# Optimization experiments

Hardware: AMD Instinct MI355X
Metric: run time of the kernel (lower is better)

Reference implementation:

```python
import jax, jax.numpy as jnp
import numpy as np

HALF_LOG_2PI = 0.5 * float(np.log(2.0 * np.pi))


def setup_inputs() -> dict:
    key = jax.random.key(0)
    k1, k2 = jax.random.split(key)
    N, D = 16384, 2048
    x = jax.random.normal(k1, (N, D), dtype=jnp.float32)
    raw_params = jax.random.normal(k2, (2 * D,), dtype=jnp.float32)
    # chain spanning tree: edges (i, i+1) for i in 0..D-2  -> shape [D-1, 2]
    idx = jnp.arange(D - 1, dtype=jnp.int64)
    edges = jnp.stack([idx, idx + 1], axis=1)
    return {"x": x, "raw_params": raw_params, "edges": edges}


def reference(x, raw_params, edges):
    # x: [N, D] float; raw_params: [2D] float; edges: [E, 2] int
    D = x.shape[1]
    means = jnp.tanh(raw_params[:D]) * 2.0               # [D]
    stds = jax.nn.softplus(raw_params[D:]) + 1e-6         # [D]
    # Each edge (i, j) contributes logN(x_i) + logN(x_j); equivalently each
    # feature k contributes deg(k) * logN(x_k), deg = endpoint multiplicity.
    deg = jnp.zeros((D,), dtype=x.dtype).at[edges.reshape(-1)].add(1.0)  # [D]
    z = (x - means) / stds                                # [N, D]
    logp = -0.5 * z * z - jnp.log(stds) - HALF_LOG_2PI    # [N, D]
    return logp @ deg                                     # [N]
```

## Files before the change

kernel.cpp:

```cpp
#include <hip/hip_runtime.h>
#include <math.h>

#define HALF_LOG_2PI_F 0.9189385332046727f

typedef float f32x4 __attribute__((ext_vector_type(4)));

__global__ void clt_prep_kernel(const float* __restrict__ rp,
                                const int* __restrict__ edges,
                                float* __restrict__ A,
                                float* __restrict__ B,
                                float* __restrict__ csum,
                                int D, int E) {
    extern __shared__ float sdeg[];
    for (int k = threadIdx.x; k < D; k += blockDim.x) sdeg[k] = 0.0f;
    __syncthreads();
    for (int e = threadIdx.x; e < E; e += blockDim.x) {
        atomicAdd(&sdeg[edges[2 * e]], 1.0f);
        atomicAdd(&sdeg[edges[2 * e + 1]], 1.0f);
    }
    __syncthreads();
    float local_c = 0.0f;
    for (int k = threadIdx.x; k < D; k += blockDim.x) {
        float m = tanhf(rp[k]) * 2.0f;
        float sx = rp[D + k];
        float s = fmaxf(sx, 0.0f) + log1pf(expf(-fabsf(sx))) + 1e-6f;
        float inv_s2 = 1.0f / (s * s);
        float deg = sdeg[k];
        A[k] = deg * (-0.5f * inv_s2);
        B[k] = deg * (m * inv_s2);
        local_c += deg * (-0.5f * m * m * inv_s2 - logf(s) - HALF_LOG_2PI_F);
    }
    __shared__ float wsum[16];
    for (int off = 32; off > 0; off >>= 1)
        local_c += __shfl_down(local_c, off, 64);
    if ((threadIdx.x & 63) == 0) wsum[threadIdx.x >> 6] = local_c;
    __syncthreads();
    if (threadIdx.x == 0) {
        float t = 0.0f;
        int nw = (blockDim.x + 63) >> 6;
        for (int w = 0; w < nw; ++w) t += wsum[w];
        *csum = t;
    }
}

template <int NI>
__global__ __launch_bounds__(256, 8) void clt_slice(
        const float* __restrict__ x,
        const float* __restrict__ A,
        const float* __restrict__ B,
        const float* __restrict__ csum,
        float* __restrict__ out,
        int D, int N, int nblocks) {
    const int lane = threadIdx.x & 63;
    const int w = threadIdx.x >> 6;
    const int colbase = w * (NI * 64);

    const f32x4* Av = (const f32x4*)A;
    const f32x4* Bv = (const f32x4*)B;
    f32x4 a4[NI], b4[NI];
#pragma unroll
    for (int i = 0; i < NI; ++i) {
        a4[i] = Av[colbase + i * 64 + lane];
        b4[i] = Bv[colbase + i * 64 + lane];
    }
    const float c = *csum;

    __shared__ float lds[8][4];

    for (int rb = blockIdx.x; rb * 8 < N; rb += nblocks) {
        const int r0 = rb * 8;
#pragma unroll 2
        for (int r = 0; r < 8; ++r) {
            const f32x4* xv = (const f32x4*)(x + (size_t)(r0 + r) * (size_t)D)
                              + colbase;
            float p = 0.0f, q = 0.0f;
#pragma unroll
            for (int i = 0; i < NI; ++i) {
                f32x4 xq = xv[i * 64 + lane];
                p += xq.x * fmaf(a4[i].x, xq.x, b4[i].x);
                q += xq.y * fmaf(a4[i].y, xq.y, b4[i].y);
                p += xq.z * fmaf(a4[i].z, xq.z, b4[i].z);
                q += xq.w * fmaf(a4[i].w, xq.w, b4[i].w);
            }
            float acc = p + q;
#pragma unroll
            for (int off = 32; off > 0; off >>= 1)
                acc += __shfl_down(acc, off, 64);
            if (lane == 0) lds[r][w] = acc;
        }
        __syncthreads();
        if (threadIdx.x < 8) {
            out[r0 + threadIdx.x] = lds[threadIdx.x][0] + lds[threadIdx.x][1]
                                  + lds[threadIdx.x][2] + lds[threadIdx.x][3]
                                  + c;
        }
        __syncthreads();
    }
}

__global__ __launch_bounds__(256) void clt_row_generic(
        const float* __restrict__ x,
        const float* __restrict__ A,
        const float* __restrict__ B,
        const float* __restrict__ csum,
        float* __restrict__ out,
        int D) {
    const int row = blockIdx.x;
    float acc = 0.0f;
    for (int k = threadIdx.x; k < D; k += blockDim.x) {
        float xs = x[(size_t)row * (size_t)D + k];
        acc += xs * fmaf(A[k], xs, B[k]);
    }
    for (int off = 32; off > 0; off >>= 1)
        acc += __shfl_down(acc, off, 64);
    __shared__ float wsum[4];
    if ((threadIdx.x & 63) == 0) wsum[threadIdx.x >> 6] = acc;
    __syncthreads();
    if (threadIdx.x == 0)
        out[row] = wsum[0] + wsum[1] + wsum[2] + wsum[3] + *csum;
}

extern "C" void kernel_launch(void* const* d_in, const int* in_sizes, int n_in,
                              void* d_out, int out_size, void* d_ws, size_t ws_size,
                              hipStream_t stream) {
    const float* x     = (const float*)d_in[0];
    const float* rp    = (const float*)d_in[1];
    const int*   edges = (const int*)d_in[2];
    float* out = (float*)d_out;

    const int D = in_sizes[1] / 2;
    const int E = in_sizes[2] / 2;
    const int N = out_size;

    float* A    = (float*)d_ws;
    float* B    = A + D;
    float* csum = B + D;

    clt_prep_kernel<<<1, 1024, D * sizeof(float), stream>>>(rp, edges, A, B, csum, D, E);

    const int NI = D / 1024;
    if (N % 8 == 0 && D == NI * 1024 && (NI == 1 || NI == 2 || NI == 4)) {
        int nblocks = N / 8;
        if (nblocks > 2048) nblocks = 2048;
        switch (NI) {
            case 1:  clt_slice<1><<<nblocks, 256, 0, stream>>>(x, A, B, csum, out, D, N, nblocks); break;
            case 2:  clt_slice<2><<<nblocks, 256, 0, stream>>>(x, A, B, csum, out, D, N, nblocks); break;
            default: clt_slice<4><<<nblocks, 256, 0, stream>>>(x, A, B, csum, out, D, N, nblocks); break;
        }
    } else {
        clt_row_generic<<<N, 256, 0, stream>>>(x, A, B, csum, out, D);
    }
}
```

Baseline: 36.28 us.

## Issue all row loads upfront per block and drop grid-stride loop

The main kernel now launches one block per 8-row group instead of a capped grid-stride loop. Each thread loads all 8 rows' vectors into registers before computing, then runs the 8 shuffle reductions interleaved. This raises memory-level parallelism so the kernel hides HBM latency better on a bandwidth-bound 128MB read. The cost is more registers (launch bounds occupancy hint removed) and possibly lower occupancy.

Result: faster. 35.51 us (-2.1%).

```diff
diff --git a/kernel.cpp b/kernel.cpp
--- a/kernel.cpp
+++ b/kernel.cpp
@@ -44,16 +44,17 @@
 }
 
 template <int NI>
-__global__ __launch_bounds__(256, 8) void clt_slice(
+__global__ __launch_bounds__(256) void clt_slice8(
         const float* __restrict__ x,
         const float* __restrict__ A,
         const float* __restrict__ B,
         const float* __restrict__ csum,
         float* __restrict__ out,
-        int D, int N, int nblocks) {
+        int D) {
     const int lane = threadIdx.x & 63;
     const int w = threadIdx.x >> 6;
     const int colbase = w * (NI * 64);
+    const int rowstride = D >> 2;
 
     const f32x4* Av = (const f32x4*)A;
     const f32x4* Bv = (const f32x4*)B;
@@ -65,36 +66,49 @@
     }
     const float c = *csum;
 
+    const int r0 = blockIdx.x * 8;
+    const f32x4* xv = (const f32x4*)(x + (size_t)r0 * (size_t)D)
+                      + colbase + lane;
+
+    f32x4 xr[8][NI];
+#pragma unroll
+    for (int r = 0; r < 8; ++r)
+#pragma unroll
+        for (int i = 0; i < NI; ++i)
+            xr[r][i] = xv[(size_t)r * rowstride + i * 64];
+
+    float acc[8];
+#pragma unroll
+    for (int r = 0; r < 8; ++r) {
+        float p = 0.0f, q = 0.0f;
+#pragma unroll
+        for (int i = 0; i < NI; ++i) {
+            f32x4 xq = xr[r][i];
+            p += xq.x * fmaf(a4[i].x, xq.x, b4[i].x);
+            q += xq.y * fmaf(a4[i].y, xq.y, b4[i].y);
+            p += xq.z * fmaf(a4[i].z, xq.z, b4[i].z);
+            q += xq.w * fmaf(a4[i].w, xq.w, b4[i].w);
+        }
+        acc[r] = p + q;
+    }
+
+#pragma unroll
+    for (int off = 32; off > 0; off >>= 1) {
+#pragma unroll
+        for (int r = 0; r < 8; ++r)
+            acc[r] += __shfl_down(acc[r], off, 64);
+    }
+
     __shared__ float lds[8][4];
-
-    for (int rb = blockIdx.x; rb * 8 < N; rb += nblocks) {
-        const int r0 = rb * 8;
-#pragma unroll 2
-        for (int r = 0; r < 8; ++r) {
-            const f32x4* xv = (const f32x4*)(x + (size_t)(r0 + r) * (size_t)D)
-                              + colbase;
-            float p = 0.0f, q = 0.0f;
+    if (lane == 0) {
 #pragma unroll
-            for (int i = 0; i < NI; ++i) {
-                f32x4 xq = xv[i * 64 + lane];
-                p += xq.x * fmaf(a4[i].x, xq.x, b4[i].x);
-                q += xq.y * fmaf(a4[i].y, xq.y, b4[i].y);
-                p += xq.z * fmaf(a4[i].z, xq.z, b4[i].z);
-                q += xq.w * fmaf(a4[i].w, xq.w, b4[i].w);
-            }
-            float acc = p + q;
-#pragma unroll
-            for (int off = 32; off > 0; off >>= 1)
-                acc += __shfl_down(acc, off, 64);
-            if (lane == 0) lds[r][w] = acc;
-        }
-        __syncthreads();
-        if (threadIdx.x < 8) {
-            out[r0 + threadIdx.x] = lds[threadIdx.x][0] + lds[threadIdx.x][1]
-                                  + lds[threadIdx.x][2] + lds[threadIdx.x][3]
-                                  + c;
-        }
-        __syncthreads();
+        for (int r = 0; r < 8; ++r) lds[r][w] = acc[r];
+    }
+    __syncthreads();
+    if (threadIdx.x < 8) {
+        out[r0 + threadIdx.x] = lds[threadIdx.x][0] + lds[threadIdx.x][1]
+                              + lds[threadIdx.x][2] + lds[threadIdx.x][3]
+                              + c;
     }
 }
 
@@ -140,12 +154,11 @@
 
     const int NI = D / 1024;
     if (N % 8 == 0 && D == NI * 1024 && (NI == 1 || NI == 2 || NI == 4)) {
-        int nblocks = N / 8;
-        if (nblocks > 2048) nblocks = 2048;
+        const int nblocks = N / 8;
         switch (NI) {
-            case 1:  clt_slice<1><<<nblocks, 256, 0, stream>>>(x, A, B, csum, out, D, N, nblocks); break;
-            case 2:  clt_slice<2><<<nblocks, 256, 0, stream>>>(x, A, B, csum, out, D, N, nblocks); break;
-            default: clt_slice<4><<<nblocks, 256, 0, stream>>>(x, A, B, csum, out, D, N, nblocks); break;
+            case 1:  clt_slice8<1><<<nblocks, 256, 0, stream>>>(x, A, B, csum, out, D); break;
+            case 2:  clt_slice8<2><<<nblocks, 256, 0, stream>>>(x, A, B, csum, out, D); break;
+            default: clt_slice8<4><<<nblocks, 256, 0, stream>>>(x, A, B, csum, out, D); break;
         }
     } else {
         clt_row_generic<<<N, 256, 0, stream>>>(x, A, B, csum, out, D);
```
